# Kernel optimization log

Hardware: AMD Instinct MI355X
Metric: run time of the kernel (lower is better)

The kernel has to match this reference:

```python
import jax, jax.numpy as jnp
import numpy as np


def setup_inputs() -> dict:
    key = jax.random.key(0)
    k1, k2 = jax.random.split(key)
    B, F_in, N, F_out = 4, 64, 8192, 64
    x = jax.random.normal(k1, (B, F_in, N), dtype=jnp.float32)
    stdv = 1.0 / np.sqrt(F_out)
    weight = jax.random.uniform(k2, (F_in, F_out), dtype=jnp.float32, minval=-stdv, maxval=stdv)
    return {"x": x, "weight": weight}


def reference(x, weight):
    # x: [B, F_in, N], weight: [F_in, F_out]
    x_t = jnp.transpose(x, (0, 2, 1))              # [B, N, F_in]
    support = jnp.einsum('bnf,fo->bno', x_t, weight)  # [B, N, F_out]
    adj = jnp.einsum('bnf,bfm->bnm', x_t, x)       # [B, N, N]
    adj = jax.nn.softmax(adj, axis=2)
    out = jnp.einsum('bnm,bmo->bno', adj, support) # [B, N, F_out]
    return jnp.transpose(out, (0, 2, 1))           # [B, F_out, N]
```

## Files before the change

kernel.cpp:

```cpp
#include <hip/hip_runtime.h>

#define BATCH 4
#define NPTS  8192
#define FDIM  64
#define BK    64
#define NT    (NPTS / BK)

typedef _Float16 half_t;
typedef half_t half8  __attribute__((ext_vector_type(8)));
typedef half_t half2v __attribute__((ext_vector_type(2)));
typedef float  f32x4  __attribute__((ext_vector_type(4)));
typedef float  f32x16 __attribute__((ext_vector_type(16)));
typedef unsigned uint4v __attribute__((ext_vector_type(4)));
typedef unsigned uint2v __attribute__((ext_vector_type(2)));

__device__ inline unsigned pkrtz(float a, float b) {
    return __builtin_bit_cast(unsigned, __builtin_amdgcn_cvt_pkrtz(a, b));
}
__device__ inline half2v h2(unsigned u) { return __builtin_bit_cast(half2v, u); }

__device__ inline uint2v plswap(unsigned a, unsigned b) {
    return __builtin_amdgcn_permlane32_swap(a, b, false, false);
}

__global__ __launch_bounds__(128) void prep_kernel(
    const float* __restrict__ x, const float* __restrict__ w,
    half_t* __restrict__ q, half_t* __restrict__ vt, float* __restrict__ nrm)
{
    __shared__ float wl[FDIM * FDIM];
    int t = threadIdx.x;
    #pragma unroll
    for (int i = 0; i < (FDIM * FDIM) / 128; ++i)
        wl[i * 128 + t] = w[i * 128 + t];
    __syncthreads();

    int gid = blockIdx.x * 128 + t;
    int b = gid >> 13;
    int n = gid & (NPTS - 1);
    const float* xb = x + (size_t)b * FDIM * NPTS + n;

    float acc[FDIM];
    #pragma unroll
    for (int o = 0; o < FDIM; ++o) acc[o] = 0.0f;
    float nr = 0.0f;

    half8* qrow = (half8*)(q + (size_t)gid * FDIM);
    #pragma unroll
    for (int f8 = 0; f8 < 8; ++f8) {
        half8 h;
        #pragma unroll
        for (int j = 0; j < 8; ++j) {
            int f = f8 * 8 + j;
            float xv = xb[(size_t)f * NPTS];
            nr += xv * xv;
            h[j] = (half_t)xv;
            const f32x4* wr = (const f32x4*)&wl[f * FDIM];
            #pragma unroll
            for (int o4 = 0; o4 < FDIM / 4; ++o4) {
                f32x4 wv = wr[o4];
                acc[o4*4+0] += xv * wv[0];
                acc[o4*4+1] += xv * wv[1];
                acc[o4*4+2] += xv * wv[2];
                acc[o4*4+3] += xv * wv[3];
            }
        }
        qrow[f8] = h;
    }
    nrm[gid] = nr * 1.44269504f;
    half_t* vb = vt + (size_t)b * FDIM * NPTS + n;
    #pragma unroll
    for (int o = 0; o < FDIM; ++o)
        vb[(size_t)o * NPTS] = (half_t)acc[o];
}

template<int SPLIT>
__global__ __launch_bounds__(256, 2) void flash_kernel(
    const half_t* __restrict__ qk, const half_t* __restrict__ vt,
    const float* __restrict__ nrm, float* __restrict__ out,
    float* __restrict__ part, float* __restrict__ lbuf)
{
    constexpr int TPS   = NT / SPLIT;
    constexpr int TOTAL = BATCH * SPLIT * (NPTS / 256);

    __shared__ half_t kl[2][BK * FDIM];
    __shared__ half_t vl[2][BK * FDIM];

    int t    = threadIdx.x;
    int lane = t & 63;
    int l31  = lane & 31;
    int hi   = lane >> 5;
    int w    = t >> 6;

    int blk0 = blockIdx.x;
    int blk  = (blk0 & 7) * (TOTAL / 8) + (blk0 >> 3);
    int qc   = blk & 31;
    int rest = blk >> 5;
    int s    = rest & (SPLIT - 1);
    int b    = rest / SPLIT;
    int qw   = qc * 256 + w * 64;

    const half_t* kg = qk + (size_t)b * NPTS * FDIM;
    const half_t* vg = vt + (size_t)b * FDIM * NPTS;

    half8 qf[2][4];
    #pragma unroll
    for (int qt = 0; qt < 2; ++qt)
        #pragma unroll
        for (int c = 0; c < 4; ++c) {
            qf[qt][c] = *(const half8*)(kg + (size_t)(qw + qt*32 + l31) * FDIM + c*16 + hi*8);
            qf[qt][c] = qf[qt][c] * (half_t)1.44269504f;
        }

    float m2[2];
    #pragma unroll
    for (int qt = 0; qt < 2; ++qt)
        m2[qt] = nrm[(size_t)b * NPTS + qw + qt*32 + l31];

    int r0 = t >> 3, g0 = t & 7;
    int r1 = r0 + 32;
    int li0 = r0 * FDIM + ((g0 ^ (r0 & 7)) * 8);
    int li1 = r1 * FDIM + ((g0 ^ (r1 & 7)) * 8);

    int kb0 = s * TPS * BK;
    half8 s0 = *(const half8*)(kg + (size_t)(kb0 + r0) * FDIM + g0*8);
    half8 s1 = *(const half8*)(kg + (size_t)(kb0 + r1) * FDIM + g0*8);
    half8 s2 = *(const half8*)(vg + (size_t)r0 * NPTS + kb0 + g0*8);
    half8 s3 = *(const half8*)(vg + (size_t)r1 * NPTS + kb0 + g0*8);

    f32x16 O[2][2];
    #pragma unroll
    for (int ot = 0; ot < 2; ++ot)
        #pragma unroll
        for (int qt = 0; qt < 2; ++qt)
            #pragma unroll
            for (int r = 0; r < 16; ++r) O[ot][qt][r] = 0.0f;
    float lsum[2] = {0.0f, 0.0f};

    for (int tt = 0; tt < TPS; ++tt) {
        half_t* klb = kl[tt & 1];
        half_t* vlb = vl[tt & 1];
        *(half8*)(klb + li0) = s0;
        *(half8*)(klb + li1) = s1;
        *(half8*)(vlb + li0) = s2;
        *(half8*)(vlb + li1) = s3;
        if (tt + 1 < TPS) {
            int kb = kb0 + (tt + 1) * BK;
            s0 = *(const half8*)(kg + (size_t)(kb + r0) * FDIM + g0*8);
            s1 = *(const half8*)(kg + (size_t)(kb + r1) * FDIM + g0*8);
            s2 = *(const half8*)(vg + (size_t)r0 * NPTS + kb + g0*8);
            s3 = *(const half8*)(vg + (size_t)r1 * NPTS + kb + g0*8);
        }
        __syncthreads();

        #pragma unroll
        for (int ct = 0; ct < 2; ++ct) {
            f32x16 S[2];
            #pragma unroll
            for (int r = 0; r < 16; ++r) { S[0][r] = -m2[0]; S[1][r] = -m2[1]; }
            int krow = ct * 32 + l31;
            #pragma unroll
            for (int c = 0; c < 4; ++c) {
                half8 kf = *(const half8*)(klb + krow * FDIM + (((2*c + hi) ^ (krow & 7)) * 8));
                S[0] = __builtin_amdgcn_mfma_f32_32x32x16_f16(kf, qf[0][c], S[0], 0, 0, 0);
                S[1] = __builtin_amdgcn_mfma_f32_32x32x16_f16(kf, qf[1][c], S[1], 0, 0, 0);
            }

            unsigned pk[2][8];
            #pragma unroll
            for (int qt = 0; qt < 2; ++qt) {
                #pragma unroll
                for (int rr = 0; rr < 8; ++rr)
                    pk[qt][rr] = pkrtz(__builtin_amdgcn_exp2f(S[qt][2*rr]),
                                       __builtin_amdgcn_exp2f(S[qt][2*rr+1]));
                half2v s2v = ((h2(pk[qt][0]) + h2(pk[qt][1])) + (h2(pk[qt][2]) + h2(pk[qt][3])))
                           + ((h2(pk[qt][4]) + h2(pk[qt][5])) + (h2(pk[qt][6]) + h2(pk[qt][7])));
                lsum[qt] += (float)s2v[0] + (float)s2v[1];
            }

            #pragma unroll
            for (int ktl = 0; ktl < 2; ++ktl) {
                const int kt = ct * 2 + ktl, i0 = ktl * 4;
                half8 pb[2];
                #pragma unroll
                for (int qt = 0; qt < 2; ++qt) {
                    uint2v r02 = plswap(pk[qt][i0+0], pk[qt][i0+2]);
                    uint2v r13 = plswap(pk[qt][i0+1], pk[qt][i0+3]);
                    uint4v uu; uu[0] = r02[0]; uu[1] = r13[0]; uu[2] = r02[1]; uu[3] = r13[1];
                    pb[qt] = __builtin_bit_cast(half8, uu);
                }
                int vrow0 = l31, vrow1 = 32 + l31;
                half8 vf0 = *(const half8*)(vlb + vrow0 * FDIM + (((2*kt + hi) ^ (vrow0 & 7)) * 8));
                half8 vf1 = *(const half8*)(vlb + vrow1 * FDIM + (((2*kt + hi) ^ (vrow1 & 7)) * 8));
                O[0][0] = __builtin_amdgcn_mfma_f32_32x32x16_f16(vf0, pb[0], O[0][0], 0, 0, 0);
                O[0][1] = __builtin_amdgcn_mfma_f32_32x32x16_f16(vf0, pb[1], O[0][1], 0, 0, 0);
                O[1][0] = __builtin_amdgcn_mfma_f32_32x32x16_f16(vf1, pb[0], O[1][0], 0, 0, 0);
                O[1][1] = __builtin_amdgcn_mfma_f32_32x32x16_f16(vf1, pb[1], O[1][1], 0, 0, 0);
            }
        }
    }

    lsum[0] += __shfl_xor(lsum[0], 32);
    lsum[1] += __shfl_xor(lsum[1], 32);

    if constexpr (SPLIT == 1) {
        float inv[2] = {1.0f / lsum[0], 1.0f / lsum[1]};
        size_t ob = (size_t)b * FDIM * NPTS;
        #pragma unroll
        for (int qt = 0; qt < 2; ++qt)
            #pragma unroll
            for (int ot = 0; ot < 2; ++ot)
                #pragma unroll
                for (int r = 0; r < 16; ++r) {
                    int o = ot*32 + (r & 3) + 8*(r >> 2) + 4*hi;
                    out[ob + (size_t)o * NPTS + qw + qt*32 + l31] = O[ot][qt][r] * inv[qt];
                }
    } else {
        float* pbase = part + (size_t)(s * BATCH + b) * FDIM * NPTS;
        #pragma unroll
        for (int qt = 0; qt < 2; ++qt)
            #pragma unroll
            for (int ot = 0; ot < 2; ++ot)
                #pragma unroll
                for (int r = 0; r < 16; ++r) {
                    int o = ot*32 + (r & 3) + 8*(r >> 2) + 4*hi;
                    pbase[(size_t)o * NPTS + qw + qt*32 + l31] = O[ot][qt][r];
                }
        if (hi == 0) {
            float* lb = lbuf + (size_t)(s * BATCH + b) * NPTS + qw;
            lb[l31]      = lsum[0];
            lb[32 + l31] = lsum[1];
        }
    }
}

template<int SPLIT>
__global__ __launch_bounds__(256) void combine_kernel(
    const float* __restrict__ part, const float* __restrict__ lbuf,
    float* __restrict__ out)
{
    int gid  = blockIdx.x * 256 + threadIdx.x;
    int q4   = gid & (NPTS/4 - 1);
    int rest = gid >> 11;
    int b    = rest >> 6;
    size_t ro = (size_t)rest * NPTS + (size_t)q4 * 4;

    f32x4 acc = {0,0,0,0}, ls = {0,0,0,0};
    #pragma unroll
    for (int s = 0; s < SPLIT; ++s) {
        acc += *(const f32x4*)(part + (size_t)s * BATCH * FDIM * NPTS + ro);
        ls  += *(const f32x4*)(lbuf + (size_t)(s * BATCH + b) * NPTS + (size_t)q4 * 4);
    }
    *(f32x4*)(out + ro) = acc / ls;
}

extern "C" void kernel_launch(void* const* d_in, const int* in_sizes, int n_in,
                              void* d_out, int out_size, void* d_ws, size_t ws_size,
                              hipStream_t stream) {
    (void)in_sizes; (void)n_in; (void)out_size;
    const float* x = (const float*)d_in[0];
    const float* w = (const float*)d_in[1];
    float* out = (float*)d_out;

    const size_t qelems = (size_t)BATCH * NPTS * FDIM;
    half_t* q  = (half_t*)d_ws;
    half_t* vt = q + qelems;
    float* nrm = (float*)((char*)d_ws + 2 * qelems * sizeof(half_t));
    float* part = nrm + (size_t)BATCH * NPTS;

    const size_t part_elems = (size_t)BATCH * FDIM * NPTS;
    const size_t l_elems    = (size_t)BATCH * NPTS;
    const size_t base_bytes = 2 * qelems * sizeof(half_t) + (size_t)BATCH * NPTS * sizeof(float);
    const size_t per_split  = (part_elems + l_elems) * sizeof(float);

    int split = 1;
    if (ws_size >= base_bytes + 4 * per_split)      split = 4;
    else if (ws_size >= base_bytes + 2 * per_split) split = 2;
    float* lbuf = part + (size_t)split * part_elems;

    prep_kernel<<<(BATCH * NPTS) / 128, 128, 0, stream>>>(x, w, q, vt, nrm);

    if (split == 4) {
        flash_kernel<4><<<BATCH * 4 * (NPTS / 256), 256, 0, stream>>>(q, vt, nrm, out, part, lbuf);
        combine_kernel<4><<<(BATCH * FDIM * NPTS) / 4 / 256, 256, 0, stream>>>(part, lbuf, out);
    } else if (split == 2) {
        flash_kernel<2><<<BATCH * 2 * (NPTS / 256), 256, 0, stream>>>(q, vt, nrm, out, part, lbuf);
        combine_kernel<2><<<(BATCH * FDIM * NPTS) / 4 / 256, 256, 0, stream>>>(part, lbuf, out);
    } else {
        flash_kernel<1><<<BATCH * 1 * (NPTS / 256), 256, 0, stream>>>(q, vt, nrm, out, nullptr, nullptr);
    }
}
```

Before: 96.91 us.

## Store K in MFMA-fragment layout and load K fragments directly from global

The prep kernel now writes the fp16 key matrix in a tiled layout that matches the MFMA operand fragment order, in 64-row blocks. The flash kernel drops the K shared-memory staging buffer and instead loads K fragments straight into registers from global memory, prefetching the next tile's fragments right after each MFMA use. This removes LDS writes and reads for K and halves LDS use, which may raise occupancy. In exchange it adds register pressure and relies on cache hits for the K reloads each wave repeats.

```diff
diff --git a/kernel.cpp b/kernel.cpp
--- a/kernel.cpp
+++ b/kernel.cpp
@@ -25,7 +25,7 @@
 
 __global__ __launch_bounds__(128) void prep_kernel(
     const float* __restrict__ x, const float* __restrict__ w,
-    half_t* __restrict__ q, half_t* __restrict__ vt, float* __restrict__ nrm)
+    half_t* __restrict__ ka, half_t* __restrict__ vt, float* __restrict__ nrm)
 {
     __shared__ float wl[FDIM * FDIM];
     int t = threadIdx.x;
@@ -44,7 +44,7 @@
     for (int o = 0; o < FDIM; ++o) acc[o] = 0.0f;
     float nr = 0.0f;
 
-    half8* qrow = (half8*)(q + (size_t)gid * FDIM);
+    half_t* kab = ka + (size_t)(gid >> 6) * 4096 + (size_t)(gid & 63) * 8;
     #pragma unroll
     for (int f8 = 0; f8 < 8; ++f8) {
         half8 h;
@@ -64,7 +64,7 @@
                 acc[o4*4+3] += xv * wv[3];
             }
         }
-        qrow[f8] = h;
+        *(half8*)(kab + f8 * 512) = h;
     }
     nrm[gid] = nr * 1.44269504f;
     half_t* vb = vt + (size_t)b * FDIM * NPTS + n;
@@ -82,7 +82,6 @@
     constexpr int TPS   = NT / SPLIT;
     constexpr int TOTAL = BATCH * SPLIT * (NPTS / 256);
 
-    __shared__ half_t kl[2][BK * FDIM];
     __shared__ half_t vl[2][BK * FDIM];
 
     int t    = threadIdx.x;
@@ -102,12 +101,13 @@
     const half_t* kg = qk + (size_t)b * NPTS * FDIM;
     const half_t* vg = vt + (size_t)b * FDIM * NPTS;
 
+    const half_t* qgb = kg + (size_t)(qw >> 6) * 4096 + (size_t)l31 * 8;
     half8 qf[2][4];
     #pragma unroll
     for (int qt = 0; qt < 2; ++qt)
         #pragma unroll
         for (int c = 0; c < 4; ++c) {
-            qf[qt][c] = *(const half8*)(kg + (size_t)(qw + qt*32 + l31) * FDIM + c*16 + hi*8);
+            qf[qt][c] = *(const half8*)(qgb + (c*2 + hi) * 512 + qt * 256);
             qf[qt][c] = qf[qt][c] * (half_t)1.44269504f;
         }
 
@@ -122,11 +122,19 @@
     int li1 = r1 * FDIM + ((g0 ^ (r1 & 7)) * 8);
 
     int kb0 = s * TPS * BK;
-    half8 s0 = *(const half8*)(kg + (size_t)(kb0 + r0) * FDIM + g0*8);
-    half8 s1 = *(const half8*)(kg + (size_t)(kb0 + r1) * FDIM + g0*8);
     half8 s2 = *(const half8*)(vg + (size_t)r0 * NPTS + kb0 + g0*8);
     half8 s3 = *(const half8*)(vg + (size_t)r1 * NPTS + kb0 + g0*8);
 
+    half8 kf[2][4];
+    {
+        const half_t* kgb = kg + (size_t)(kb0 >> 6) * 4096 + (size_t)l31 * 8;
+        #pragma unroll
+        for (int ct = 0; ct < 2; ++ct)
+            #pragma unroll
+            for (int c = 0; c < 4; ++c)
+                kf[ct][c] = *(const half8*)(kgb + (c*2 + hi) * 512 + ct * 256);
+    }
+
     f32x16 O[2][2];
     #pragma unroll
     for (int ot = 0; ot < 2; ++ot)
@@ -137,32 +145,32 @@
     float lsum[2] = {0.0f, 0.0f};
 
     for (int tt = 0; tt < TPS; ++tt) {
-        half_t* klb = kl[tt & 1];
         half_t* vlb = vl[tt & 1];
-        *(half8*)(klb + li0) = s0;
-        *(half8*)(klb + li1) = s1;
         *(half8*)(vlb + li0) = s2;
         *(half8*)(vlb + li1) = s3;
         if (tt + 1 < TPS) {
             int kb = kb0 + (tt + 1) * BK;
-            s0 = *(const half8*)(kg + (size_t)(kb + r0) * FDIM + g0*8);
-            s1 = *(const half8*)(kg + (size_t)(kb + r1) * FDIM + g0*8);
             s2 = *(const half8*)(vg + (size_t)r0 * NPTS + kb + g0*8);
             s3 = *(const half8*)(vg + (size_t)r1 * NPTS + kb + g0*8);
         }
         __syncthreads();
 
+        const half_t* kgbn = kg + (size_t)((kb0 + (tt + 1) * BK) >> 6) * 4096 + (size_t)l31 * 8;
+
         #pragma unroll
         for (int ct = 0; ct < 2; ++ct) {
             f32x16 S[2];
             #pragma unroll
             for (int r = 0; r < 16; ++r) { S[0][r] = -m2[0]; S[1][r] = -m2[1]; }
-            int krow = ct * 32 + l31;
             #pragma unroll
             for (int c = 0; c < 4; ++c) {
-                half8 kf = *(const half8*)(klb + krow * FDIM + (((2*c + hi) ^ (krow & 7)) * 8));
-                S[0] = __builtin_amdgcn_mfma_f32_32x32x16_f16(kf, qf[0][c], S[0], 0, 0, 0);
-                S[1] = __builtin_amdgcn_mfma_f32_32x32x16_f16(kf, qf[1][c], S[1], 0, 0, 0);
+                S[0] = __builtin_amdgcn_mfma_f32_32x32x16_f16(kf[ct][c], qf[0][c], S[0], 0, 0, 0);
+                S[1] = __builtin_amdgcn_mfma_f32_32x32x16_f16(kf[ct][c], qf[1][c], S[1], 0, 0, 0);
+            }
+            if (tt + 1 < TPS) {
+                #pragma unroll
+                for (int c = 0; c < 4; ++c)
+                    kf[ct][c] = *(const half8*)(kgbn + (c*2 + hi) * 512 + ct * 256);
             }
 
             unsigned pk[2][8];
@@ -262,8 +270,8 @@
     float* out = (float*)d_out;
 
     const size_t qelems = (size_t)BATCH * NPTS * FDIM;
-    half_t* q  = (half_t*)d_ws;
-    half_t* vt = q + qelems;
+    half_t* ka = (half_t*)d_ws;
+    half_t* vt = ka + qelems;
     float* nrm = (float*)((char*)d_ws + 2 * qelems * sizeof(half_t));
     float* part = nrm + (size_t)BATCH * NPTS;
 
@@ -277,15 +285,15 @@
     else if (ws_size >= base_bytes + 2 * per_split) split = 2;
     float* lbuf = part + (size_t)split * part_elems;
 
-    prep_kernel<<<(BATCH * NPTS) / 128, 128, 0, stream>>>(x, w, q, vt, nrm);
+    prep_kernel<<<(BATCH * NPTS) / 128, 128, 0, stream>>>(x, w, ka, vt, nrm);
 
     if (split == 4) {
-        flash_kernel<4><<<BATCH * 4 * (NPTS / 256), 256, 0, stream>>>(q, vt, nrm, out, part, lbuf);
+        flash_kernel<4><<<BATCH * 4 * (NPTS / 256), 256, 0, stream>>>(ka, vt, nrm, out, part, lbuf);
         combine_kernel<4><<<(BATCH * FDIM * NPTS) / 4 / 256, 256, 0, stream>>>(part, lbuf, out);
     } else if (split == 2) {
-        flash_kernel<2><<<BATCH * 2 * (NPTS / 256), 256, 0, stream>>>(q, vt, nrm, out, part, lbuf);
+        flash_kernel<2><<<BATCH * 2 * (NPTS / 256), 256, 0, stream>>>(ka, vt, nrm, out, part, lbuf);
         combine_kernel<2><<<(BATCH * FDIM * NPTS) / 4 / 256, 256, 0, stream>>>(part, lbuf, out);
     } else {
-        flash_kernel<1><<<BATCH * 1 * (NPTS / 256), 256, 0, stream>>>(q, vt, nrm, out, nullptr, nullptr);
-    }
-}
+        flash_kernel<1><<<BATCH * 1 * (NPTS / 256), 256, 0, stream>>>(ka, vt, nrm, out, nullptr, nullptr);
+    }
+}
```

Measured after the change: 95.80 us. About the same (-1.1%).
